# Performance work log

Measured on AMD Instinct MI355X. Metric: run time of the kernel, lower is better.

## Reference

```python
import jax, jax.numpy as jnp
import numpy as np

B, C_IN, C_OUT, H, W, W_DIM, K = 4, 64, 64, 512, 512, 512, 3
LRELU_SLOPE = 0.2
ACT_GAIN = np.sqrt(2.0).astype(np.float32)  # lrelu def_gain
CONV_CLAMP = 256.0


def setup_inputs() -> dict:
    key = jax.random.key(0)
    ks = jax.random.split(key, 5)
    return {
        "x": jax.random.normal(ks[0], (B, C_IN, H, W), dtype=jnp.float32),
        "ws": jax.random.normal(ks[1], (B, W_DIM), dtype=jnp.float32),
        "noise": jax.random.normal(ks[2], (B, 1, H, W), dtype=jnp.float32),
        "affine_weight": jax.random.normal(ks[3], (C_IN, W_DIM), dtype=jnp.float32),
        "affine_bias": jnp.ones((C_IN,), dtype=jnp.float32),
        "conv_weight": jax.random.normal(ks[4], (C_OUT, C_IN, K, K), dtype=jnp.float32),
        "bias": jnp.zeros((C_OUT,), dtype=jnp.float32),
    }


def reference(x, ws, noise, affine_weight, affine_bias, conv_weight, bias):
    b, c_in, h, w_sp = x.shape
    c_out, _, kh, kw = conv_weight.shape
    w_dim = ws.shape[1]

    # Affine (FullyConnectedLayer with equalized LR: weight_gain = 1/sqrt(w_dim), bias_init=1)
    styles = ws @ (affine_weight.T * np.float32(1.0 / np.sqrt(w_dim))) + affine_bias  # [b, c_in]

    # Modulate per-sample weights: w = weight[None] * styles
    wmod = conv_weight[None] * styles[:, None, :, None, None]  # [b, c_out, c_in, kh, kw]

    # Demodulation coefficients
    demod = jax.lax.rsqrt(jnp.sum(jnp.square(wmod), axis=(2, 3, 4)) + 1e-8)  # [b, c_out]
    wmod = wmod * demod[:, :, None, None, None]

    # Fused grouped conv: groups = batch (conv2d_resample, up=down=1, flip_weight=True -> correlation)
    xg = x.reshape(1, b * c_in, h, w_sp)
    wg = wmod.reshape(b * c_out, c_in, kh, kw)
    pad = kh // 2
    y = jax.lax.conv_general_dilated(
        xg, wg, window_strides=(1, 1), padding=[(pad, pad), (pad, pad)],
        dimension_numbers=("NCHW", "OIHW", "NCHW"), feature_group_count=b)
    y = y.reshape(b, c_out, h, w_sp)

    # Noise add (broadcast over channels)
    y = y + noise

    # bias_act: bias + lrelu * act_gain, then clamp (conv_clamp * gain, gain=1)
    y = y + bias[None, :, None, None]
    y = jnp.where(y >= 0, y, LRELU_SLOPE * y) * ACT_GAIN
    y = jnp.clip(y, -CONV_CLAMP, CONV_CLAMP)
    return y
```

## Files before the change

### kernel.cpp

```cpp
#include <hip/hip_runtime.h>
#include <math.h>

#define HH 512
#define WW 512
#define HW (HH * WW)
#define PW 514
#define PPIX (PW * PW)

#define A_U 36864
#define B_U 11776
#define LDS_BYTES ((A_U + 2 * B_U) * 2)

typedef short bf16x8 __attribute__((ext_vector_type(8)));
typedef float f32x4 __attribute__((ext_vector_type(4)));

__device__ __forceinline__ ushort f2bf(float f) {
    union { float f; uint u; } c; c.f = f;
    uint u = c.u;
    return (ushort)((u + 0x7fffu + ((u >> 16) & 1u)) >> 16);
}

__device__ __forceinline__ uint cvtpk(float a, float b) {
    uint r;
    asm("v_cvt_pk_bf16_f32 %0, %1, %2" : "=v"(r) : "v"(a), "v"(b));
    return r;
}

__global__ void k_styles(const float* __restrict__ wsv, const float* __restrict__ aw,
                         const float* __restrict__ ab, float* __restrict__ styles) {
    int bid = blockIdx.x;
    int b = bid >> 6, ci = bid & 63;
    int l = threadIdx.x;
    const float* wrow = wsv + b * 512;
    const float* arow = aw + ci * 512;
    float s = 0.f;
    #pragma unroll
    for (int j = 0; j < 8; ++j)
        s += wrow[l + 64 * j] * arow[l + 64 * j];
    #pragma unroll
    for (int off = 32; off; off >>= 1)
        s += __shfl_xor(s, off, 64);
    if (l == 0)
        styles[b * 64 + ci] = s * 0.044194173824159216f + ab[ci];
}

__global__ void k_wmod(const float* __restrict__ cw, const float* __restrict__ styles,
                       ushort* __restrict__ wb) {
    int b = blockIdx.x >> 6, co = blockIdx.x & 63;
    int ci = threadIdx.x;
    float st = styles[b * 64 + ci];
    const float* wp = cw + (co * 64 + ci) * 9;
    float wv[9];
    float ss = 0.f;
    #pragma unroll
    for (int k = 0; k < 9; ++k) { wv[k] = wp[k] * st; ss += wv[k] * wv[k]; }
    #pragma unroll
    for (int off = 32; off; off >>= 1)
        ss += __shfl_xor(ss, off, 64);
    float dm = 1.0f / sqrtf(ss + 1e-8f);
    int cisw = ((((ci >> 3) ^ co) & 7) << 3) | (ci & 7);
    #pragma unroll
    for (int k = 0; k < 9; ++k)
        wb[((size_t)(b * 64 + co) * 9 + k) * 64 + cisw] = f2bf(wv[k] * dm);
}

__global__ __launch_bounds__(256) void k_xpose(
    const float* __restrict__ x, ushort* __restrict__ xp) {
    const int t = threadIdx.x;
    const int bid = blockIdx.x;

    if (bid >= 8192) {
        int id = (bid - 8192) * 256 + t;
        if (id >= 4 * 2052) return;
        int b = id / 2052, r = id % 2052;
        int gyp, gxp;
        if (r < 514)       { gyp = 0;        gxp = r; }
        else if (r < 1028) { gyp = 513;      gxp = r - 514; }
        else if (r < 1540) { gyp = r - 1027; gxp = 0; }
        else               { gyp = r - 1539; gxp = 513; }
        ushort* p = xp + (((size_t)b * PW + gyp) * PW + gxp) * 64;
        uint4 z = make_uint4(0, 0, 0, 0);
        #pragma unroll
        for (int i = 0; i < 8; ++i) *(uint4*)(p + i * 8) = z;
        return;
    }

    __shared__ ushort lt[128 * 68];
    const int gxt = bid & 3;
    const int gy  = (bid >> 2) & 511;
    const int b   = bid >> 11;

    const float* xb = x + (size_t)b * 64 * HW + (size_t)gy * WW + gxt * 128;
    const int ci0 = 8 * (t >> 5);
    const int gxc = t & 31;

    f32x4 v[8];
    #pragma unroll
    for (int j = 0; j < 8; ++j)
        v[j] = *(const f32x4*)(xb + (size_t)(ci0 + j) * HW + gxc * 4);

    #pragma unroll
    for (int p = 0; p < 4; ++p) {
        int px = gxc * 4 + p;
        int rowp = ((px & 3) * 32 + (px >> 2)) * 68;
        #pragma unroll
        for (int cg = 0; cg < 2; ++cg) {
            uint lo = cvtpk(v[4 * cg + 0][p], v[4 * cg + 1][p]);
            uint hi = cvtpk(v[4 * cg + 2][p], v[4 * cg + 3][p]);
            *(uint2*)&lt[rowp + ci0 + 4 * cg] = make_uint2(lo, hi);
        }
    }
    __syncthreads();

    const int px = t >> 1, half = t & 1;
    const int rowp = ((px & 3) * 32 + (px >> 2)) * 68 + half * 32;
    uint4 o0 = *(uint4*)&lt[rowp + 0];
    uint4 o1 = *(uint4*)&lt[rowp + 8];
    uint4 o2 = *(uint4*)&lt[rowp + 16];
    uint4 o3 = *(uint4*)&lt[rowp + 24];
    ushort* dst = xp + (((size_t)b * PW + (gy + 1)) * PW + (gxt * 128 + px + 1)) * 64
                     + half * 32;
    *(uint4*)(dst + 0)  = o0;
    *(uint4*)(dst + 8)  = o1;
    *(uint4*)(dst + 16) = o2;
    *(uint4*)(dst + 24) = o3;
}

__device__ __forceinline__ void stage_b(ushort* lds, const ushort* __restrict__ xpb,
                                        int p, int band, int ct, int w, int lane) {
    const int ty = band * 8;
    const int tx = ct * 16;
    for (int j = w; j < 23; j += 8) {
        int c = j * 64 + lane;
        int c2 = c < 1439 ? c : 1439;
        int cig = c2 & 7;
        int pxl = c2 >> 3;
        int row = pxl / 18;
        int lcol = pxl - row * 18;
        int gsrc = cig ^ (lcol & 7);
        const ushort* src = xpb + ((size_t)(ty + row) * PW + (tx + lcol)) * 64 + gsrc * 8;
        __builtin_amdgcn_global_load_lds(
            (const __attribute__((address_space(1))) unsigned int*)src,
            (__attribute__((address_space(3))) unsigned int*)&lds[A_U + p * B_U + j * 512],
            16, 0, 0);
    }
}

__global__ __launch_bounds__(512) void k_conv(
    const ushort* __restrict__ xp,
    const ushort* __restrict__ wb,
    const float* __restrict__ noise,
    const float* __restrict__ bias,
    float* __restrict__ out) {
    extern __shared__ __align__(16) ushort lds[];

    const int t = threadIdx.x;
    const int w = t >> 6;
    const int lane = t & 63;
    const int blk = blockIdx.x;
    const int b = blk >> 6;
    const int band = blk & 63;

    const ushort* xpb = xp + (size_t)b * PPIX * 64;
    const ushort* wA  = wb + (size_t)b * 64 * 576;

    for (int j = w; j < 72; j += 8) {
        const ushort* src = wA + j * 512 + lane * 8;
        __builtin_amdgcn_global_load_lds(
            (const __attribute__((address_space(1))) unsigned int*)src,
            (__attribute__((address_space(3))) unsigned int*)&lds[j * 512],
            16, 0, 0);
    }
    stage_b(lds, xpb, 0, band, 0, w, lane);
    asm volatile("s_waitcnt vmcnt(0)" ::: "memory");
    __syncthreads();

    const int lr = lane & 15;
    const int lq = lane >> 4;
    const int wm = w >> 2;
    const int wn = w & 3;

    int aidx[2][2];
    #pragma unroll
    for (int m = 0; m < 2; ++m)
        #pragma unroll
        for (int kb = 0; kb < 2; ++kb)
            aidx[m][kb] = ((2 * wm + m) * 16 + lr) * 576 + ((((kb << 2) | lq) ^ (lr & 7)) << 3);

    int bidx[2][3];
    #pragma unroll
    for (int i = 0; i < 2; ++i)
        #pragma unroll
        for (int dx = 0; dx < 3; ++dx) {
            int lcol = lr + dx;
            bidx[i][dx] = ((2 * wn + i) * 18 + lcol) * 64 + ((lq * 8) ^ ((lcol & 7) << 3));
        }

    f32x4 bv[2];
    #pragma unroll
    for (int m = 0; m < 2; ++m)
        bv[m] = *(const f32x4*)&bias[(2 * wm + m) * 16 + lq * 4];
    const float* nz = noise + (size_t)b * HW;
    const int ty = band * 8;

    int p = 0;
    for (int it = 0; it < 32; ++it) {
        const int tx = it * 16;
        const int gx = tx + lr;

        if (it < 31) stage_b(lds, xpb, p ^ 1, band, it + 1, w, lane);

        float nv[2];
        int gyv[2];
        #pragma unroll
        for (int i = 0; i < 2; ++i) {
            gyv[i] = ty + 2 * wn + i;
            nv[i] = nz[gyv[i] * WW + gx];
        }

        const ushort* bufp = &lds[A_U + p * B_U];
        f32x4 acc[2][2];
        #pragma unroll
        for (int m = 0; m < 2; ++m)
            #pragma unroll
            for (int i = 0; i < 2; ++i) acc[m][i] = (f32x4){0.f, 0.f, 0.f, 0.f};

        #pragma unroll
        for (int dy = 0; dy < 3; ++dy) {
            #pragma unroll
            for (int dx = 0; dx < 3; ++dx) {
                #pragma unroll
                for (int kb = 0; kb < 2; ++kb) {
                    const int off = dy * 3 + dx;
                    bf16x8 afr[2], bfr[2];
                    #pragma unroll
                    for (int m = 0; m < 2; ++m)
                        afr[m] = *(const bf16x8*)&lds[aidx[m][kb] + off * 64];
                    #pragma unroll
                    for (int i = 0; i < 2; ++i) {
                        int idx = (bidx[i][dx] + dy * (18 * 64)) ^ (kb << 5);
                        bfr[i] = *(const bf16x8*)&bufp[idx];
                    }
                    #pragma unroll
                    for (int m = 0; m < 2; ++m)
                        #pragma unroll
                        for (int i = 0; i < 2; ++i)
                            acc[m][i] = __builtin_amdgcn_mfma_f32_16x16x32_bf16(
                                afr[m], bfr[i], acc[m][i], 0, 0, 0);
                }
            }
        }

        asm volatile("s_waitcnt vmcnt(0)" ::: "memory");
        __syncthreads();

        #pragma unroll
        for (int m = 0; m < 2; ++m) {
            #pragma unroll
            for (int i = 0; i < 2; ++i) {
                #pragma unroll
                for (int rg2 = 0; rg2 < 4; ++rg2) {
                    int co = (2 * wm + m) * 16 + lq * 4 + rg2;
                    float y = acc[m][i][rg2] + nv[i] + bv[m][rg2];
                    y = (y >= 0.f ? y : 0.2f * y) * 1.41421356237f;
                    y = fminf(fmaxf(y, -256.f), 256.f);
                    out[((size_t)(b * 64 + co) * HH + gyv[i]) * WW + gx] = y;
                }
            }
        }
        p ^= 1;
    }
}

extern "C" void kernel_launch(void* const* d_in, const int* in_sizes, int n_in,
                              void* d_out, int out_size, void* d_ws, size_t ws_size,
                              hipStream_t stream) {
    const float* x     = (const float*)d_in[0];
    const float* wsv   = (const float*)d_in[1];
    const float* noise = (const float*)d_in[2];
    const float* aw    = (const float*)d_in[3];
    const float* ab    = (const float*)d_in[4];
    const float* cw    = (const float*)d_in[5];
    const float* bias  = (const float*)d_in[6];
    float* out = (float*)d_out;

    float*  styles = (float*)d_ws;
    ushort* wb16   = (ushort*)((char*)d_ws + 1024);
    ushort* xpad   = (ushort*)((char*)d_ws + (1 << 20));

    hipFuncSetAttribute((const void*)k_conv,
                        hipFuncAttributeMaxDynamicSharedMemorySize, LDS_BYTES);

    k_styles<<<256, 64, 0, stream>>>(wsv, aw, ab, styles);
    k_wmod<<<256, 64, 0, stream>>>(cw, styles, wb16);
    k_xpose<<<8225, 256, 0, stream>>>(x, xpad);
    k_conv<<<256, 512, LDS_BYTES, stream>>>(xpad, wb16, noise, bias, out);
}
```

Before: 253.5 us.

## Hold modulated weights in registers and enlarge conv tile to 16 rows

```diff
diff --git a/kernel.cpp b/kernel.cpp
--- a/kernel.cpp
+++ b/kernel.cpp
@@ -7,9 +7,8 @@
 #define PW 514
 #define PPIX (PW * PW)
 
-#define A_U 36864
-#define B_U 11776
-#define LDS_BYTES ((A_U + 2 * B_U) * 2)
+#define B_U 20992
+#define LDS_BYTES (2 * B_U * 2)
 
 typedef short bf16x8 __attribute__((ext_vector_type(8)));
 typedef float f32x4 __attribute__((ext_vector_type(4)));
@@ -58,10 +57,9 @@
     for (int off = 32; off; off >>= 1)
         ss += __shfl_xor(ss, off, 64);
     float dm = 1.0f / sqrtf(ss + 1e-8f);
-    int cisw = ((((ci >> 3) ^ co) & 7) << 3) | (ci & 7);
     #pragma unroll
     for (int k = 0; k < 9; ++k)
-        wb[((size_t)(b * 64 + co) * 9 + k) * 64 + cisw] = f2bf(wv[k] * dm);
+        wb[((size_t)(b * 64 + co) * 9 + k) * 64 + ci] = f2bf(wv[k] * dm);
 }
 
 __global__ __launch_bounds__(256) void k_xpose(
@@ -126,26 +124,6 @@
     *(uint4*)(dst + 24) = o3;
 }
 
-__device__ __forceinline__ void stage_b(ushort* lds, const ushort* __restrict__ xpb,
-                                        int p, int band, int ct, int w, int lane) {
-    const int ty = band * 8;
-    const int tx = ct * 16;
-    for (int j = w; j < 23; j += 8) {
-        int c = j * 64 + lane;
-        int c2 = c < 1439 ? c : 1439;
-        int cig = c2 & 7;
-        int pxl = c2 >> 3;
-        int row = pxl / 18;
-        int lcol = pxl - row * 18;
-        int gsrc = cig ^ (lcol & 7);
-        const ushort* src = xpb + ((size_t)(ty + row) * PW + (tx + lcol)) * 64 + gsrc * 8;
-        __builtin_amdgcn_global_load_lds(
-            (const __attribute__((address_space(1))) unsigned int*)src,
-            (__attribute__((address_space(3))) unsigned int*)&lds[A_U + p * B_U + j * 512],
-            16, 0, 0);
-    }
-}
-
 __global__ __launch_bounds__(512) void k_conv(
     const ushort* __restrict__ xp,
     const ushort* __restrict__ wb,
@@ -157,73 +135,108 @@
     const int t = threadIdx.x;
     const int w = t >> 6;
     const int lane = t & 63;
-    const int blk = blockIdx.x;
-    const int b = blk >> 6;
-    const int band = blk & 63;
-
-    const ushort* xpb = xp + (size_t)b * PPIX * 64;
-    const ushort* wA  = wb + (size_t)b * 64 * 576;
-
-    for (int j = w; j < 72; j += 8) {
-        const ushort* src = wA + j * 512 + lane * 8;
-        __builtin_amdgcn_global_load_lds(
-            (const __attribute__((address_space(1))) unsigned int*)src,
-            (__attribute__((address_space(3))) unsigned int*)&lds[j * 512],
-            16, 0, 0);
-    }
-    stage_b(lds, xpb, 0, band, 0, w, lane);
-    asm volatile("s_waitcnt vmcnt(0)" ::: "memory");
-    __syncthreads();
-
     const int lr = lane & 15;
     const int lq = lane >> 4;
     const int wm = w >> 2;
     const int wn = w & 3;
 
-    int aidx[2][2];
-    #pragma unroll
-    for (int m = 0; m < 2; ++m)
-        #pragma unroll
-        for (int kb = 0; kb < 2; ++kb)
-            aidx[m][kb] = ((2 * wm + m) * 16 + lr) * 576 + ((((kb << 2) | lq) ^ (lr & 7)) << 3);
-
-    int bidx[2][3];
-    #pragma unroll
-    for (int i = 0; i < 2; ++i)
+    const int blk = blockIdx.x;
+    const int b = blk >> 6;
+    const int band = (blk >> 1) & 31;
+    const int ch = blk & 1;
+    const int ty = band * 16;
+    const int tx0 = ch * 256;
+
+    const ushort* xpb = xp + (size_t)b * PPIX * 64;
+
+    const ushort* wA = wb + (size_t)b * 64 * 576;
+    bf16x8 areg[2][9][2];
+    #pragma unroll
+    for (int m = 0; m < 2; ++m) {
+        const ushort* pco = wA + (wm * 32 + m * 16 + lr) * 576 + lq * 8;
+        #pragma unroll
+        for (int off = 0; off < 9; ++off)
+            #pragma unroll
+            for (int kb = 0; kb < 2; ++kb)
+                areg[m][off][kb] = *(const bf16x8*)(pco + off * 64 + kb * 32);
+    }
+
+    int soff[6];
+    #pragma unroll
+    for (int jj = 0; jj < 6; ++jj) {
+        int j = w + jj * 8;
+        if (j < 41) {
+            int c = j * 64 + lane;
+            int c2 = c < 2591 ? c : 2591;
+            int cig = c2 & 7;
+            int pxl = c2 >> 3;
+            int row = pxl / 18;
+            int lcol = pxl - row * 18;
+            int gsrc = cig ^ (lcol & 7);
+            soff[jj] = ((ty + row) * PW + lcol) * 64 + gsrc * 8;
+        } else soff[jj] = 0;
+    }
+
+    int bidx[4][3];
+    #pragma unroll
+    for (int i = 0; i < 4; ++i)
         #pragma unroll
         for (int dx = 0; dx < 3; ++dx) {
             int lcol = lr + dx;
-            bidx[i][dx] = ((2 * wn + i) * 18 + lcol) * 64 + ((lq * 8) ^ ((lcol & 7) << 3));
+            bidx[i][dx] = ((wn * 4 + i) * 18 + lcol) * 64 + ((lq * 8) ^ ((lcol & 7) << 3));
         }
 
     f32x4 bv[2];
     #pragma unroll
     for (int m = 0; m < 2; ++m)
-        bv[m] = *(const f32x4*)&bias[(2 * wm + m) * 16 + lq * 4];
+        bv[m] = *(const f32x4*)&bias[wm * 32 + m * 16 + lq * 4];
     const float* nz = noise + (size_t)b * HW;
-    const int ty = band * 8;
+
+    #pragma unroll
+    for (int jj = 0; jj < 6; ++jj) {
+        int j = w + jj * 8;
+        if (j < 41)
+            __builtin_amdgcn_global_load_lds(
+                (const __attribute__((address_space(1))) unsigned int*)(xpb + soff[jj] + tx0 * 64),
+                (__attribute__((address_space(3))) unsigned int*)&lds[j * 512],
+                16, 0, 0);
+    }
+    asm volatile("s_waitcnt vmcnt(0)" ::: "memory");
+    __syncthreads();
 
     int p = 0;
-    for (int it = 0; it < 32; ++it) {
-        const int tx = it * 16;
+    for (int it = 0; it < 16; ++it) {
+        const int tx = tx0 + it * 16;
         const int gx = tx + lr;
 
-        if (it < 31) stage_b(lds, xpb, p ^ 1, band, it + 1, w, lane);
-
-        float nv[2];
-        int gyv[2];
-        #pragma unroll
-        for (int i = 0; i < 2; ++i) {
-            gyv[i] = ty + 2 * wn + i;
+        if (it < 15) {
+            #pragma unroll
+            for (int jj = 0; jj < 6; ++jj) {
+                int j = w + jj * 8;
+                if (j < 41)
+                    __builtin_amdgcn_global_load_lds(
+                        (const __attribute__((address_space(1))) unsigned int*)
+                            (xpb + soff[jj] + (tx + 16) * 64),
+                        (__attribute__((address_space(3))) unsigned int*)
+                            &lds[(p ^ 1) * B_U + j * 512],
+                        16, 0, 0);
+            }
+        }
+
+        float nv[4];
+        int gyv[4];
+        #pragma unroll
+        for (int i = 0; i < 4; ++i) {
+            gyv[i] = ty + wn * 4 + i;
             nv[i] = nz[gyv[i] * WW + gx];
         }
 
-        const ushort* bufp = &lds[A_U + p * B_U];
-        f32x4 acc[2][2];
+        const ushort* bufp = &lds[p * B_U];
+        f32x4 acc[2][4];
         #pragma unroll
         for (int m = 0; m < 2; ++m)
             #pragma unroll
-            for (int i = 0; i < 2; ++i) acc[m][i] = (f32x4){0.f, 0.f, 0.f, 0.f};
+            for (int i = 0; i < 4; ++i) acc[m][i] = (f32x4){0.f, 0.f, 0.f, 0.f};
 
         #pragma unroll
         for (int dy = 0; dy < 3; ++dy) {
@@ -232,21 +245,17 @@
                 #pragma unroll
                 for (int kb = 0; kb < 2; ++kb) {
                     const int off = dy * 3 + dx;
-                    bf16x8 afr[2], bfr[2];
+                    bf16x8 bfr[4];
                     #pragma unroll
-                    for (int m = 0; m < 2; ++m)
-                        afr[m] = *(const bf16x8*)&lds[aidx[m][kb] + off * 64];
-                    #pragma unroll
-                    for (int i = 0; i < 2; ++i) {
-                        int idx = (bidx[i][dx] + dy * (18 * 64)) ^ (kb << 5);
-                        bfr[i] = *(const bf16x8*)&bufp[idx];
-                    }
+                    for (int i = 0; i < 4; ++i)
+                        bfr[i] = *(const bf16x8*)
+                            &bufp[(bidx[i][dx] + dy * (18 * 64)) ^ (kb << 5)];
                     #pragma unroll
                     for (int m = 0; m < 2; ++m)
                         #pragma unroll
-                        for (int i = 0; i < 2; ++i)
+                        for (int i = 0; i < 4; ++i)
                             acc[m][i] = __builtin_amdgcn_mfma_f32_16x16x32_bf16(
-                                afr[m], bfr[i], acc[m][i], 0, 0, 0);
+                                areg[m][off][kb], bfr[i], acc[m][i], 0, 0, 0);
                 }
             }
         }
@@ -257,11 +266,11 @@
         #pragma unroll
         for (int m = 0; m < 2; ++m) {
             #pragma unroll
-            for (int i = 0; i < 2; ++i) {
+            for (int i = 0; i < 4; ++i) {
                 #pragma unroll
-                for (int rg2 = 0; rg2 < 4; ++rg2) {
-                    int co = (2 * wm + m) * 16 + lq * 4 + rg2;
-                    float y = acc[m][i][rg2] + nv[i] + bv[m][rg2];
+                for (int rg = 0; rg < 4; ++rg) {
+                    int co = wm * 32 + m * 16 + lq * 4 + rg;
+                    float y = acc[m][i][rg] + nv[i] + bv[m][rg];
                     y = (y >= 0.f ? y : 0.2f * y) * 1.41421356237f;
                     y = fminf(fmaxf(y, -256.f), 256.f);
                     out[((size_t)(b * 64 + co) * HH + gyv[i]) * WW + gx] = y;
```

After: 381.1 us. +50.3%, slower.

## Switch conv to 32x32x16 MFMA with wider column tiles and 256-thread blocks

Applied to the files above, without the earlier changes.

```diff
diff --git a/kernel.cpp b/kernel.cpp
--- a/kernel.cpp
+++ b/kernel.cpp
@@ -8,11 +8,12 @@
 #define PPIX (PW * PW)
 
 #define A_U 36864
-#define B_U 11776
+#define B_U 22016
 #define LDS_BYTES ((A_U + 2 * B_U) * 2)
 
 typedef short bf16x8 __attribute__((ext_vector_type(8)));
-typedef float f32x4 __attribute__((ext_vector_type(4)));
+typedef float f32x4  __attribute__((ext_vector_type(4)));
+typedef float f32x16 __attribute__((ext_vector_type(16)));
 
 __device__ __forceinline__ ushort f2bf(float f) {
     union { float f; uint u; } c; c.f = f;
@@ -126,27 +127,7 @@
     *(uint4*)(dst + 24) = o3;
 }
 
-__device__ __forceinline__ void stage_b(ushort* lds, const ushort* __restrict__ xpb,
-                                        int p, int band, int ct, int w, int lane) {
-    const int ty = band * 8;
-    const int tx = ct * 16;
-    for (int j = w; j < 23; j += 8) {
-        int c = j * 64 + lane;
-        int c2 = c < 1439 ? c : 1439;
-        int cig = c2 & 7;
-        int pxl = c2 >> 3;
-        int row = pxl / 18;
-        int lcol = pxl - row * 18;
-        int gsrc = cig ^ (lcol & 7);
-        const ushort* src = xpb + ((size_t)(ty + row) * PW + (tx + lcol)) * 64 + gsrc * 8;
-        __builtin_amdgcn_global_load_lds(
-            (const __attribute__((address_space(1))) unsigned int*)src,
-            (__attribute__((address_space(3))) unsigned int*)&lds[A_U + p * B_U + j * 512],
-            16, 0, 0);
-    }
-}
-
-__global__ __launch_bounds__(512) void k_conv(
+__global__ __launch_bounds__(256, 1) void k_conv(
     const ushort* __restrict__ xp,
     const ushort* __restrict__ wb,
     const float* __restrict__ noise,
@@ -157,96 +138,126 @@
     const int t = threadIdx.x;
     const int w = t >> 6;
     const int lane = t & 63;
+    const int n5 = lane & 31;
+    const int hl = lane >> 5;
     const int blk = blockIdx.x;
     const int b = blk >> 6;
     const int band = blk & 63;
+    const int ty = band * 8;
 
     const ushort* xpb = xp + (size_t)b * PPIX * 64;
     const ushort* wA  = wb + (size_t)b * 64 * 576;
 
-    for (int j = w; j < 72; j += 8) {
+    #pragma unroll
+    for (int jj = 0; jj < 18; ++jj) {
+        int j = w + jj * 4;
         const ushort* src = wA + j * 512 + lane * 8;
         __builtin_amdgcn_global_load_lds(
             (const __attribute__((address_space(1))) unsigned int*)src,
             (__attribute__((address_space(3))) unsigned int*)&lds[j * 512],
             16, 0, 0);
     }
-    stage_b(lds, xpb, 0, band, 0, w, lane);
+
+    int soff[11];
+    #pragma unroll
+    for (int jj = 0; jj < 11; ++jj) {
+        int j = w + jj * 4;
+        if (j < 43) {
+            int c = j * 64 + lane;
+            int c2 = c < 2719 ? c : 2719;
+            int cig = c2 & 7;
+            int pxl = c2 >> 3;
+            int row = pxl / 34;
+            int lcol = pxl - row * 34;
+            int gsrc = cig ^ (lcol & 7);
+            soff[jj] = ((ty + row) * PW + lcol) * 64 + gsrc * 8;
+        } else soff[jj] = 0;
+    }
+
+    #pragma unroll
+    for (int jj = 0; jj < 11; ++jj) {
+        int j = w + jj * 4;
+        if (j < 43)
+            __builtin_amdgcn_global_load_lds(
+                (const __attribute__((address_space(1))) unsigned int*)(xpb + soff[jj]),
+                (__attribute__((address_space(3))) unsigned int*)&lds[A_U + j * 512],
+                16, 0, 0);
+    }
     asm volatile("s_waitcnt vmcnt(0)" ::: "memory");
     __syncthreads();
 
-    const int lr = lane & 15;
-    const int lq = lane >> 4;
-    const int wm = w >> 2;
-    const int wn = w & 3;
-
-    int aidx[2][2];
-    #pragma unroll
-    for (int m = 0; m < 2; ++m)
-        #pragma unroll
-        for (int kb = 0; kb < 2; ++kb)
-            aidx[m][kb] = ((2 * wm + m) * 16 + lr) * 576 + ((((kb << 2) | lq) ^ (lr & 7)) << 3);
+    int aidx[2];
+    #pragma unroll
+    for (int mt = 0; mt < 2; ++mt)
+        aidx[mt] = (mt * 32 + n5) * 576 + ((hl ^ (n5 & 7)) << 3);
 
     int bidx[2][3];
+    const int brow = 2 * w + (n5 >> 4);
     #pragma unroll
     for (int i = 0; i < 2; ++i)
         #pragma unroll
         for (int dx = 0; dx < 3; ++dx) {
-            int lcol = lr + dx;
-            bidx[i][dx] = ((2 * wn + i) * 18 + lcol) * 64 + ((lq * 8) ^ ((lcol & 7) << 3));
-        }
-
-    f32x4 bv[2];
-    #pragma unroll
-    for (int m = 0; m < 2; ++m)
-        bv[m] = *(const f32x4*)&bias[(2 * wm + m) * 16 + lq * 4];
+            int lcol = i * 16 + (n5 & 15) + dx;
+            bidx[i][dx] = (brow * 34 + lcol) * 64 + ((hl ^ (lcol & 7)) << 3);
+        }
+
     const float* nz = noise + (size_t)b * HW;
-    const int ty = band * 8;
+    const int orow = ty + brow;
 
     int p = 0;
-    for (int it = 0; it < 32; ++it) {
-        const int tx = it * 16;
-        const int gx = tx + lr;
-
-        if (it < 31) stage_b(lds, xpb, p ^ 1, band, it + 1, w, lane);
+    for (int it = 0; it < 16; ++it) {
+        const int tx = it * 32;
+
+        if (it < 15) {
+            #pragma unroll
+            for (int jj = 0; jj < 11; ++jj) {
+                int j = w + jj * 4;
+                if (j < 43)
+                    __builtin_amdgcn_global_load_lds(
+                        (const __attribute__((address_space(1))) unsigned int*)
+                            (xpb + soff[jj] + (tx + 32) * 64),
+                        (__attribute__((address_space(3))) unsigned int*)
+                            &lds[A_U + (p ^ 1) * B_U + j * 512],
+                        16, 0, 0);
+            }
+        }
 
         float nv[2];
-        int gyv[2];
-        #pragma unroll
-        for (int i = 0; i < 2; ++i) {
-            gyv[i] = ty + 2 * wn + i;
-            nv[i] = nz[gyv[i] * WW + gx];
-        }
+        #pragma unroll
+        for (int i = 0; i < 2; ++i)
+            nv[i] = nz[orow * WW + tx + i * 16 + (n5 & 15)];
 
         const ushort* bufp = &lds[A_U + p * B_U];
-        f32x4 acc[2][2];
-        #pragma unroll
-        for (int m = 0; m < 2; ++m)
+        f32x16 acc[2][2];
+        #pragma unroll
+        for (int mt = 0; mt < 2; ++mt)
             #pragma unroll
-            for (int i = 0; i < 2; ++i) acc[m][i] = (f32x4){0.f, 0.f, 0.f, 0.f};
+            for (int i = 0; i < 2; ++i)
+                acc[mt][i] = (f32x16){0.f,0.f,0.f,0.f,0.f,0.f,0.f,0.f,
+                                      0.f,0.f,0.f,0.f,0.f,0.f,0.f,0.f};
 
         #pragma unroll
         for (int dy = 0; dy < 3; ++dy) {
             #pragma unroll
             for (int dx = 0; dx < 3; ++dx) {
+                const int off = dy * 3 + dx;
                 #pragma unroll
-                for (int kb = 0; kb < 2; ++kb) {
-                    const int off = dy * 3 + dx;
+                for (int kb = 0; kb < 4; ++kb) {
                     bf16x8 afr[2], bfr[2];
                     #pragma unroll
-                    for (int m = 0; m < 2; ++m)
-                        afr[m] = *(const bf16x8*)&lds[aidx[m][kb] + off * 64];
+                    for (int mt = 0; mt < 2; ++mt)
+                        afr[mt] = *(const bf16x8*)
+                            &lds[(aidx[mt] + off * 64) ^ (kb << 4)];
                     #pragma unroll
-                    for (int i = 0; i < 2; ++i) {
-                        int idx = (bidx[i][dx] + dy * (18 * 64)) ^ (kb << 5);
-                        bfr[i] = *(const bf16x8*)&bufp[idx];
-                    }
+                    for (int i = 0; i < 2; ++i)
+                        bfr[i] = *(const bf16x8*)
+                            &bufp[(bidx[i][dx] + dy * (34 * 64)) ^ (kb << 4)];
                     #pragma unroll
-                    for (int m = 0; m < 2; ++m)
+                    for (int mt = 0; mt < 2; ++mt)
                         #pragma unroll
                         for (int i = 0; i < 2; ++i)
-                            acc[m][i] = __builtin_amdgcn_mfma_f32_16x16x32_bf16(
-                                afr[m], bfr[i], acc[m][i], 0, 0, 0);
+                            acc[mt][i] = __builtin_amdgcn_mfma_f32_32x32x16_bf16(
+                                afr[mt], bfr[i], acc[mt][i], 0, 0, 0);
                 }
             }
         }
@@ -255,16 +266,17 @@
         __syncthreads();
 
         #pragma unroll
-        for (int m = 0; m < 2; ++m) {
+        for (int mt = 0; mt < 2; ++mt) {
             #pragma unroll
             for (int i = 0; i < 2; ++i) {
+                const int ocol = tx + i * 16 + (n5 & 15);
                 #pragma unroll
-                for (int rg2 = 0; rg2 < 4; ++rg2) {
-                    int co = (2 * wm + m) * 16 + lq * 4 + rg2;
-                    float y = acc[m][i][rg2] + nv[i] + bv[m][rg2];
+                for (int reg = 0; reg < 16; ++reg) {
+                    int co = mt * 32 + (reg & 3) + 8 * (reg >> 2) + 4 * hl;
+                    float y = acc[mt][i][reg] + nv[i] + bias[co];
                     y = (y >= 0.f ? y : 0.2f * y) * 1.41421356237f;
                     y = fminf(fmaxf(y, -256.f), 256.f);
-                    out[((size_t)(b * 64 + co) * HH + gyv[i]) * WW + gx] = y;
+                    out[((size_t)(b * 64 + co) * HH + orow) * WW + ocol] = y;
                 }
             }
         }
@@ -294,5 +306,5 @@
     k_styles<<<256, 64, 0, stream>>>(wsv, aw, ab, styles);
     k_wmod<<<256, 64, 0, stream>>>(cw, styles, wb16);
     k_xpose<<<8225, 256, 0, stream>>>(x, xpad);
-    k_conv<<<256, 512, LDS_BYTES, stream>>>(xpad, wb16, noise, bias, out);
-}
+    k_conv<<<256, 256, LDS_BYTES, stream>>>(xpad, wb16, noise, bias, out);
+}
```

Result: slower. 260.5 us (+2.7%).
